# Optimization experiments

Measured on AMD Instinct MI355X. Metric: run time of the kernel, lower is better.

Reference implementation:

```python
import jax, jax.numpy as jnp
import numpy as np

DIM = 512
NUM_HEADS = 8
HEAD_DIM = DIM // NUM_HEADS
LN_EPS = 1e-5


def setup_inputs() -> dict:
    key = jax.random.key(0)
    k1, k2, k3 = jax.random.split(key, 3)
    x = jax.random.normal(k1, (8, DIM, 32, 32), dtype=jnp.float32)
    # torch Linear default init scale ~ 1/sqrt(fan_in); keep values sane
    w_qkv = jax.random.normal(k2, (3 * DIM, DIM), dtype=jnp.float32) * (DIM ** -0.5)
    b_qkv = jax.random.normal(k3, (3 * DIM,), dtype=jnp.float32) * 0.01
    ln_gamma = jnp.ones((DIM,), dtype=jnp.float32)
    ln_beta = jnp.zeros((DIM,), dtype=jnp.float32)
    return {"x": x, "w_qkv": w_qkv, "b_qkv": b_qkv, "ln_gamma": ln_gamma, "ln_beta": ln_beta}


def _rotate_half(t):
    t1, t2 = jnp.split(t, 2, axis=-1)
    return jnp.concatenate((-t2, t1), axis=-1)


def reference(x, w_qkv, b_qkv, ln_gamma, ln_beta):
    B, C, H, W = x.shape
    N = H * W
    nh, hd = NUM_HEADS, HEAD_DIM
    scale = hd ** -0.5

    # [B, N, C]
    xt = x.reshape(B, C, N).transpose(0, 2, 1)

    # LayerNorm over channel dim
    mu = jnp.mean(xt, axis=-1, keepdims=True)
    var = jnp.mean(jnp.square(xt - mu), axis=-1, keepdims=True)
    xn = (xt - mu) * jax.lax.rsqrt(var + LN_EPS) * ln_gamma + ln_beta

    # QKV projection: [B, N, 3C]
    qkv = xn @ w_qkv.T + b_qkv
    qkv = qkv.reshape(B, N, 3, nh, hd).transpose(2, 0, 3, 1, 4)  # [3, B, nh, N, hd]
    q, k, v = qkv[0], qkv[1], qkv[2]

    # RoPE tables
    freqs = 1.0 / (10000.0 ** (jnp.arange(0, hd, 2, dtype=jnp.float32) / hd))
    pos = jnp.arange(N, dtype=jnp.float32)
    sinusoid = jnp.einsum('i,j->ij', pos, freqs)  # [N, hd/2]
    sin = jnp.repeat(jnp.sin(sinusoid), 2, axis=-1)[None, None]  # [1,1,N,hd]
    cos = jnp.repeat(jnp.cos(sinusoid), 2, axis=-1)[None, None]

    q = q * cos + _rotate_half(q) * sin
    k = k * cos + _rotate_half(k) * sin

    # Full softmax attention: [B, nh, N, N]
    attn = jnp.einsum('bhqd,bhkd->bhqk', q, k) * scale
    attn = jax.nn.softmax(attn, axis=-1)
    out = jnp.einsum('bhqk,bhkd->bhqd', attn, v)  # [B, nh, N, hd]

    out = out.transpose(0, 2, 1, 3).reshape(B, N, C)  # [B, N, C]
    # dropout=0 (eval): identity
    return out.transpose(0, 2, 1).reshape(B, C, H, W)
```

## Files before the change

### kernel.cpp

```cpp
#include <hip/hip_runtime.h>
#include <hip/hip_bf16.h>
#include <math.h>

using bf16 = __hip_bfloat16;
typedef __attribute__((ext_vector_type(8))) short short8;
typedef __attribute__((ext_vector_type(4))) short short4_;
typedef __attribute__((ext_vector_type(4))) float floatx4;

#define C_DIM   512
#define N_TOK   1024
#define NHEAD   8
#define HDIM    64
#define LN_EPSF 1e-5f

__device__ __forceinline__ unsigned short f2b(float f) {
    union { float f; unsigned int u; } v; v.f = f;
    unsigned int r = v.u + 0x7FFFu + ((v.u >> 16) & 1u);
    return (unsigned short)(r >> 16);
}
__device__ __forceinline__ float b2f(unsigned short u) {
    union { unsigned int i; float f; } v; v.i = ((unsigned int)u) << 16; return v.f;
}

__global__ __launch_bounds__(256) void prep_kernel(
        const float* __restrict__ x, const float* __restrict__ w,
        float* __restrict__ mu, float* __restrict__ rsig,
        float* __restrict__ sc, unsigned short* __restrict__ wf) {
    __shared__ float red_s[4][64];
    __shared__ float red_q[4][64];
    const int bx = blockIdx.x;
    const int t  = threadIdx.x;
    if (bx < 128) {
        const int rl = t & 63;
        const int cg = t >> 6;
        const int r0 = bx * 64;
        const int b  = r0 >> 10;
        const int n  = (r0 & 1023) + rl;
        const float* xp = x + (size_t)b * C_DIM * N_TOK + n;
        float s = 0.f, q = 0.f;
        #pragma unroll 4
        for (int i = 0; i < 128; ++i) {
            float v = xp[(size_t)(cg * 128 + i) * N_TOK];
            s += v; q += v * v;
        }
        red_s[cg][rl] = s; red_q[cg][rl] = q;
        __syncthreads();
        if (cg == 0) {
            float S = red_s[0][rl] + red_s[1][rl] + red_s[2][rl] + red_s[3][rl];
            float Q = red_q[0][rl] + red_q[1][rl] + red_q[2][rl] + red_q[3][rl];
            float m   = S * (1.0f / C_DIM);
            float var = Q * (1.0f / C_DIM) - m * m;
            mu[r0 + rl]   = m;
            rsig[r0 + rl] = rsqrtf(var + LN_EPSF);
        }
    } else if (bx < 256) {
        const int idx = (bx - 128) * 256 + t;
        const int n = idx >> 5, f = idx & 31;
        const float fr = __expf((float)f * (-9.210340371976184f / 32.0f));
        float sv, cv;
        sincosf((float)n * fr, &sv, &cv);
        ((float2*)sc)[idx] = make_float2(sv, cv);
    } else {
        const int id   = (bx - 256) * 256 + t;
        const int lane = id & 63;
        const int ksl  = (id >> 6) & 15;
        const int j16  = id >> 10;
        const int c    = lane & 15;
        const int quad = lane >> 4;
        const float* wp = w + (size_t)(j16 * 16 + c) * C_DIM + ksl * 32 + quad * 8;
        const float4 w0 = *(const float4*)(wp);
        const float4 w1 = *(const float4*)(wp + 4);
        short8 pk;
        pk[0] = (short)f2b(w0.x); pk[1] = (short)f2b(w0.y);
        pk[2] = (short)f2b(w0.z); pk[3] = (short)f2b(w0.w);
        pk[4] = (short)f2b(w1.x); pk[5] = (short)f2b(w1.y);
        pk[6] = (short)f2b(w1.z); pk[7] = (short)f2b(w1.w);
        *(short8*)(wf + (size_t)id * 8) = pk;
    }
}

__global__ __launch_bounds__(256) void xnt_kernel(
        const float* __restrict__ x, const float* __restrict__ gamma,
        const float* __restrict__ beta, const float* __restrict__ mu,
        const float* __restrict__ rsig, unsigned short* __restrict__ xnf) {
    __shared__ short Sx[64][72];
    const int t  = threadIdx.x;
    const int c0 = blockIdx.x * 64;
    const int n0 = blockIdx.y * 64;
    const int b  = blockIdx.z;

    const int nq  = t & 15;
    const int crl = t >> 4;
    const int tok = b * N_TOK + n0 + nq * 4;
    const float4 m4 = *(const float4*)(mu + tok);
    const float4 r4 = *(const float4*)(rsig + tok);
    #pragma unroll
    for (int p = 0; p < 4; ++p) {
        const int c = c0 + p * 16 + crl;
        const float g = gamma[c], bt = beta[c];
        const float4 xv = *(const float4*)(x + (size_t)b * C_DIM * N_TOK + (size_t)c * N_TOK + n0 + nq * 4);
        Sx[nq * 4 + 0][p * 16 + crl] = (short)f2b((xv.x - m4.x) * r4.x * g + bt);
        Sx[nq * 4 + 1][p * 16 + crl] = (short)f2b((xv.y - m4.y) * r4.y * g + bt);
        Sx[nq * 4 + 2][p * 16 + crl] = (short)f2b((xv.z - m4.z) * r4.z * g + bt);
        Sx[nq * 4 + 3][p * 16 + crl] = (short)f2b((xv.w - m4.w) * r4.w * g + bt);
    }
    __syncthreads();
    const int wv   = t >> 6;
    const int lane = t & 63;
    const int cfr  = lane & 15;
    const int quad = lane >> 4;
    const int g16  = b * 64 + ((n0 >> 4) + wv);
    #pragma unroll
    for (int ks = 0; ks < 2; ++ks) {
        short8 v = *(const short8*)&Sx[wv * 16 + cfr][ks * 32 + quad * 8];
        *(short8*)(xnf + (((size_t)g16 * 16 + (c0 >> 5) + ks) * 64 + lane) * 8) = v;
    }
}

__global__ __launch_bounds__(256) void qkv_mfma_kernel(
        const unsigned short* __restrict__ xnf, const unsigned short* __restrict__ wf,
        const float* __restrict__ bias, const float* __restrict__ sc,
        unsigned short* __restrict__ qfr, unsigned short* __restrict__ kfr,
        unsigned short* __restrict__ vfr) {
    __shared__ short Es[4][64][72];

    const int t    = threadIdx.x;
    const int wv   = t >> 6;
    const int lane = t & 63;
    const int cl   = lane & 15;
    const int quad = lane >> 4;
    const int t0   = blockIdx.x * 128 + (wv & 1) * 64;
    const int j0w  = blockIdx.y * 128 + (wv >> 1) * 64;
    const int which = j0w >> 9;
    const int h     = (j0w >> 6) & 7;
    const int b     = t0 >> 10;
    const int n0q   = t0 & 1023;
    const int bh    = b * NHEAD + h;

    const unsigned short* ap = xnf + (size_t)(t0 >> 4) * 8192 + lane * 8;
    const unsigned short* bp = wf  + (size_t)(j0w >> 4) * 8192 + lane * 8;

    floatx4 acc[4][4];
    #pragma unroll
    for (int i = 0; i < 4; ++i)
        #pragma unroll
        for (int j = 0; j < 4; ++j) acc[i][j] = (floatx4){0.f, 0.f, 0.f, 0.f};

    #pragma unroll 2
    for (int kt = 0; kt < 16; ++kt) {
        short8 af[4], bfr[4];
        #pragma unroll
        for (int tt = 0; tt < 4; ++tt) af[tt]  = *(const short8*)(ap + ((size_t)tt * 16 + kt) * 512);
        #pragma unroll
        for (int jt = 0; jt < 4; ++jt) bfr[jt] = *(const short8*)(bp + ((size_t)jt * 16 + kt) * 512);
        #pragma unroll
        for (int tt = 0; tt < 4; ++tt)
            #pragma unroll
            for (int jt = 0; jt < 4; ++jt)
                acc[tt][jt] = __builtin_amdgcn_mfma_f32_16x16x32_bf16(af[tt], bfr[jt], acc[tt][jt], 0, 0, 0);
    }

    float bj[4];
    #pragma unroll
    for (int jt = 0; jt < 4; ++jt) bj[jt] = bias[j0w + jt * 16 + cl];
    #pragma unroll
    for (int tt = 0; tt < 4; ++tt)
        #pragma unroll
        for (int jt = 0; jt < 4; ++jt)
            #pragma unroll
            for (int r = 0; r < 4; ++r)
                Es[wv][tt * 16 + quad * 4 + r][jt * 16 + cl] = (short)f2b(acc[tt][jt][r] + bj[jt]);

    if (which == 2) {
        unsigned short* vfb = vfr + ((size_t)bh * 16 + (n0q >> 6)) * 4096;
        #pragma unroll
        for (int dt = 0; dt < 4; ++dt) {
            #pragma unroll
            for (int ks = 0; ks < 2; ++ks) {
                short8 pk;
                #pragma unroll
                for (int j = 0; j < 8; ++j)
                    pk[j] = Es[wv][ks * 32 + quad * 8 + j][dt * 16 + cl];
                *(short8*)(vfb + (((size_t)dt * 2 + ks) * 64 + lane) * 8) = pk;
            }
        }
    } else {
        const float oscale = (which == 0) ? 0.125f : 1.0f;
        unsigned short* base = (which == 0)
            ? qfr + ((size_t)bh * 64 + (n0q >> 4)) * 1024
            : kfr + ((size_t)bh * 16 + (n0q >> 6)) * 4096;
        #pragma unroll
        for (int mt = 0; mt < 4; ++mt) {
            const int n = n0q + mt * 16 + cl;
            const float* scp = sc + ((size_t)n * 32 + quad * 4) * 2;
            #pragma unroll
            for (int ks = 0; ks < 2; ++ks) {
                const short8 v8 = *(const short8*)&Es[wv][mt * 16 + cl][ks * 32 + quad * 8];
                const short8 p8 = *(const short8*)&Es[wv][mt * 16 + cl][(ks ^ 1) * 32 + quad * 8];
                const float* sp = scp + ks * 32;
                const float4 s0 = *(const float4*)sp;
                const float4 s1 = *(const float4*)(sp + 4);
                const float sv[4] = {s0.x, s0.z, s1.x, s1.z};
                const float cv[4] = {s0.y, s0.w, s1.y, s1.w};
                const float sgn = ks ? 1.0f : -1.0f;
                short8 pk;
                #pragma unroll
                for (int j = 0; j < 8; ++j) {
                    const int f = j >> 1;
                    const float val = b2f((unsigned short)v8[j]);
                    const float par = b2f((unsigned short)p8[j]);
                    pk[j] = (short)f2b((val * cv[f] + sgn * par * sv[f]) * oscale);
                }
                *(short8*)(base + (((size_t)mt * 2 + ks) * 64 + lane) * 8) = pk;
            }
        }
    }
}

__global__ __launch_bounds__(64, 2) void attn_mfma_kernel(
        const unsigned short* __restrict__ qfr, const unsigned short* __restrict__ kfr,
        const unsigned short* __restrict__ vfr, float* __restrict__ out) {
    __shared__ __align__(16) short Plds[2][16][72];

    const int lane = threadIdx.x;
    const int c    = lane & 15;
    const int quad = lane >> 4;
    const int i    = blockIdx.x;
    const int bh   = (i & 7) * 8 + ((i >> 3) & 7);
    const int qw   = (i >> 6) * 32;
    const int b    = bh >> 3, h = bh & 7;

    const unsigned short* qp = qfr + ((size_t)bh * 64 + (qw >> 4)) * 1024 + lane * 8;
    const unsigned short* kp = kfr + (size_t)bh * 65536 + lane * 8;
    const unsigned short* vp = vfr + (size_t)bh * 65536 + lane * 8;

    short8 qf[2][2];
    #pragma unroll
    for (int qt = 0; qt < 2; ++qt)
        #pragma unroll
        for (int ks = 0; ks < 2; ++ks)
            qf[qt][ks] = *(const short8*)(qp + ((size_t)qt * 2 + ks) * 512);

    floatx4 o_acc[2][4];
    float l_acc[2] = {0.f, 0.f};
    #pragma unroll
    for (int qt = 0; qt < 2; ++qt)
        #pragma unroll
        for (int dt = 0; dt < 4; ++dt) o_acc[qt][dt] = (floatx4){0.f, 0.f, 0.f, 0.f};

    #pragma unroll 1
    for (int kt = 0; kt < 16; ++kt) {
        const unsigned short* kb = kp + (size_t)kt * 4096;
        const unsigned short* vb = vp + (size_t)kt * 4096;
        short8 kf[4][2], vf[4][2];
        #pragma unroll
        for (int mt = 0; mt < 4; ++mt) {
            #pragma unroll
            for (int ks = 0; ks < 2; ++ks) {
                kf[mt][ks] = *(const short8*)(kb + ((size_t)mt * 2 + ks) * 512);
                vf[mt][ks] = *(const short8*)(vb + ((size_t)mt * 2 + ks) * 512);
            }
        }

        floatx4 st[2][4];
        #pragma unroll
        for (int qt = 0; qt < 2; ++qt) {
            #pragma unroll
            for (int mt = 0; mt < 4; ++mt) {
                floatx4 z = (floatx4){0.f, 0.f, 0.f, 0.f};
                z = __builtin_amdgcn_mfma_f32_16x16x32_bf16(kf[mt][0], qf[qt][0], z, 0, 0, 0);
                st[qt][mt] = __builtin_amdgcn_mfma_f32_16x16x32_bf16(kf[mt][1], qf[qt][1], z, 0, 0, 0);
            }
        }

        #pragma unroll
        for (int qt = 0; qt < 2; ++qt) {
            #pragma unroll
            for (int mt = 0; mt < 4; ++mt) {
                const float e0 = __expf(st[qt][mt][0] - 16.0f);
                const float e1 = __expf(st[qt][mt][1] - 16.0f);
                const float e2 = __expf(st[qt][mt][2] - 16.0f);
                const float e3 = __expf(st[qt][mt][3] - 16.0f);
                l_acc[qt] += (e0 + e1) + (e2 + e3);
                short4_ pk;
                pk.x = (short)f2b(e0); pk.y = (short)f2b(e1);
                pk.z = (short)f2b(e2); pk.w = (short)f2b(e3);
                *(short4_*)&Plds[qt][c][mt * 16 + quad * 4] = pk;
            }
        }

        #pragma unroll
        for (int qt = 0; qt < 2; ++qt) {
            const short8 pf0 = *(const short8*)&Plds[qt][c][quad * 8];
            const short8 pf1 = *(const short8*)&Plds[qt][c][32 + quad * 8];
            #pragma unroll
            for (int dt = 0; dt < 4; ++dt) {
                o_acc[qt][dt] = __builtin_amdgcn_mfma_f32_16x16x32_bf16(vf[dt][0], pf0, o_acc[qt][dt], 0, 0, 0);
                o_acc[qt][dt] = __builtin_amdgcn_mfma_f32_16x16x32_bf16(vf[dt][1], pf1, o_acc[qt][dt], 0, 0, 0);
            }
        }
    }

    #pragma unroll
    for (int qt = 0; qt < 2; ++qt) {
        float l = l_acc[qt];
        l += __shfl_xor(l, 16);
        l += __shfl_xor(l, 32);
        const float inv = 1.0f / l;
        const int qcol = qw + qt * 16 + c;
        #pragma unroll
        for (int dt = 0; dt < 4; ++dt) {
            #pragma unroll
            for (int r = 0; r < 4; ++r) {
                const int d = dt * 16 + quad * 4 + r;
                out[((size_t)b * C_DIM + h * HDIM + d) * N_TOK + qcol] = o_acc[qt][dt][r] * inv;
            }
        }
    }
}

extern "C" void kernel_launch(void* const* d_in, const int* in_sizes, int n_in,
                              void* d_out, int out_size, void* d_ws, size_t ws_size,
                              hipStream_t stream) {
    const float* x     = (const float*)d_in[0];
    const float* w     = (const float*)d_in[1];
    const float* bias  = (const float*)d_in[2];
    const float* gamma = (const float*)d_in[3];
    const float* beta  = (const float*)d_in[4];
    float* out = (float*)d_out;

    char* ws = (char*)d_ws;
    float* mu   = (float*)ws;
    float* rsig = (float*)(ws + 32768);
    unsigned short* qfr = (unsigned short*)(ws + 65536);
    unsigned short* kfr = (unsigned short*)(ws + 65536 + 8388608);
    unsigned short* vfr = (unsigned short*)(ws + 65536 + 16777216);
    unsigned short* xnf = (unsigned short*)(ws + 65536 + 25165824);
    unsigned short* wf  = (unsigned short*)(ws + 65536 + 33554432);
    float* sc           = (float*)(ws + 65536 + 35127296);

    hipLaunchKernelGGL(prep_kernel, dim3(640), dim3(256), 0, stream, x, w, mu, rsig, sc, wf);
    hipLaunchKernelGGL(xnt_kernel, dim3(8, 16, 8), dim3(256), 0, stream,
                       x, gamma, beta, mu, rsig, xnf);
    hipLaunchKernelGGL(qkv_mfma_kernel, dim3(64, 12), dim3(256), 0, stream,
                       xnf, wf, bias, sc, qfr, kfr, vfr);
    hipLaunchKernelGGL(attn_mfma_kernel, dim3(2048), dim3(64), 0, stream, qfr, kfr, vfr, out);
}
```

Before: 150.7 us.

## Fuse LayerNorm stats and normalize-transpose into prep kernel; raise attention occupancy hint

The separate xnt kernel is folded into the stats blocks of prep_kernel. Each block computes the mean and rstd for its 64 tokens, keeps them in shared memory, then loops over all 8 channel chunks to write the bf16 fragment layout. This removes a launch and the global mu/rsig round-trip. The cost is that only 128 blocks now do all the normalize work serially, so parallelism for that phase drops. Separately, the attention kernel's launch bounds go from 2 to 3 blocks per SM, which may force register limits or spills.

```diff
diff --git a/kernel.cpp b/kernel.cpp
--- a/kernel.cpp
+++ b/kernel.cpp
@@ -24,34 +24,69 @@
 
 __global__ __launch_bounds__(256) void prep_kernel(
         const float* __restrict__ x, const float* __restrict__ w,
-        float* __restrict__ mu, float* __restrict__ rsig,
-        float* __restrict__ sc, unsigned short* __restrict__ wf) {
-    __shared__ float red_s[4][64];
-    __shared__ float red_q[4][64];
+        const float* __restrict__ gamma, const float* __restrict__ beta,
+        float* __restrict__ sc, unsigned short* __restrict__ xnf,
+        unsigned short* __restrict__ wf) {
     const int bx = blockIdx.x;
     const int t  = threadIdx.x;
     if (bx < 128) {
-        const int rl = t & 63;
-        const int cg = t >> 6;
-        const int r0 = bx * 64;
-        const int b  = r0 >> 10;
-        const int n  = (r0 & 1023) + rl;
-        const float* xp = x + (size_t)b * C_DIM * N_TOK + n;
-        float s = 0.f, q = 0.f;
-        #pragma unroll 4
-        for (int i = 0; i < 128; ++i) {
-            float v = xp[(size_t)(cg * 128 + i) * N_TOK];
-            s += v; q += v * v;
-        }
-        red_s[cg][rl] = s; red_q[cg][rl] = q;
-        __syncthreads();
-        if (cg == 0) {
-            float S = red_s[0][rl] + red_s[1][rl] + red_s[2][rl] + red_s[3][rl];
-            float Q = red_q[0][rl] + red_q[1][rl] + red_q[2][rl] + red_q[3][rl];
-            float m   = S * (1.0f / C_DIM);
-            float var = Q * (1.0f / C_DIM) - m * m;
-            mu[r0 + rl]   = m;
-            rsig[r0 + rl] = rsqrtf(var + LN_EPSF);
+        __shared__ float red_s[4][64];
+        __shared__ float red_q[4][64];
+        __shared__ float lmu[64];
+        __shared__ float lrs[64];
+        __shared__ short Sx[64][72];
+        const int b  = bx >> 4;
+        const int n0 = (bx & 15) * 64;
+        {
+            const int rl = t & 63;
+            const int cg = t >> 6;
+            const float* xp = x + (size_t)b * C_DIM * N_TOK + n0 + rl;
+            float s = 0.f, q = 0.f;
+            #pragma unroll 4
+            for (int i = 0; i < 128; ++i) {
+                float v = xp[(size_t)(cg * 128 + i) * N_TOK];
+                s += v; q += v * v;
+            }
+            red_s[cg][rl] = s; red_q[cg][rl] = q;
+            __syncthreads();
+            if (cg == 0) {
+                float S = red_s[0][rl] + red_s[1][rl] + red_s[2][rl] + red_s[3][rl];
+                float Q = red_q[0][rl] + red_q[1][rl] + red_q[2][rl] + red_q[3][rl];
+                float m   = S * (1.0f / C_DIM);
+                float var = Q * (1.0f / C_DIM) - m * m;
+                lmu[rl] = m;
+                lrs[rl] = rsqrtf(var + LN_EPSF);
+            }
+            __syncthreads();
+        }
+        const int nq  = t & 15;
+        const int crl = t >> 4;
+        const int wv   = t >> 6;
+        const int lane = t & 63;
+        const int cfr  = lane & 15;
+        const int quad = lane >> 4;
+        const int g16  = b * 64 + (n0 >> 4) + wv;
+        const float4 m4 = *(const float4*)&lmu[nq * 4];
+        const float4 r4 = *(const float4*)&lrs[nq * 4];
+        for (int cc = 0; cc < 8; ++cc) {
+            const int c0 = cc * 64;
+            #pragma unroll
+            for (int p = 0; p < 4; ++p) {
+                const int c = c0 + p * 16 + crl;
+                const float g = gamma[c], bt = beta[c];
+                const float4 xv = *(const float4*)(x + (size_t)b * C_DIM * N_TOK + (size_t)c * N_TOK + n0 + nq * 4);
+                Sx[nq * 4 + 0][p * 16 + crl] = (short)f2b((xv.x - m4.x) * r4.x * g + bt);
+                Sx[nq * 4 + 1][p * 16 + crl] = (short)f2b((xv.y - m4.y) * r4.y * g + bt);
+                Sx[nq * 4 + 2][p * 16 + crl] = (short)f2b((xv.z - m4.z) * r4.z * g + bt);
+                Sx[nq * 4 + 3][p * 16 + crl] = (short)f2b((xv.w - m4.w) * r4.w * g + bt);
+            }
+            __syncthreads();
+            #pragma unroll
+            for (int ks = 0; ks < 2; ++ks) {
+                short8 v = *(const short8*)&Sx[wv * 16 + cfr][ks * 32 + quad * 8];
+                *(short8*)(xnf + (((size_t)g16 * 16 + cc * 2 + ks) * 64 + lane) * 8) = v;
+            }
+            __syncthreads();
         }
     } else if (bx < 256) {
         const int idx = (bx - 128) * 256 + t;
@@ -79,44 +114,6 @@
     }
 }
 
-__global__ __launch_bounds__(256) void xnt_kernel(
-        const float* __restrict__ x, const float* __restrict__ gamma,
-        const float* __restrict__ beta, const float* __restrict__ mu,
-        const float* __restrict__ rsig, unsigned short* __restrict__ xnf) {
-    __shared__ short Sx[64][72];
-    const int t  = threadIdx.x;
-    const int c0 = blockIdx.x * 64;
-    const int n0 = blockIdx.y * 64;
-    const int b  = blockIdx.z;
-
-    const int nq  = t & 15;
-    const int crl = t >> 4;
-    const int tok = b * N_TOK + n0 + nq * 4;
-    const float4 m4 = *(const float4*)(mu + tok);
-    const float4 r4 = *(const float4*)(rsig + tok);
-    #pragma unroll
-    for (int p = 0; p < 4; ++p) {
-        const int c = c0 + p * 16 + crl;
-        const float g = gamma[c], bt = beta[c];
-        const float4 xv = *(const float4*)(x + (size_t)b * C_DIM * N_TOK + (size_t)c * N_TOK + n0 + nq * 4);
-        Sx[nq * 4 + 0][p * 16 + crl] = (short)f2b((xv.x - m4.x) * r4.x * g + bt);
-        Sx[nq * 4 + 1][p * 16 + crl] = (short)f2b((xv.y - m4.y) * r4.y * g + bt);
-        Sx[nq * 4 + 2][p * 16 + crl] = (short)f2b((xv.z - m4.z) * r4.z * g + bt);
-        Sx[nq * 4 + 3][p * 16 + crl] = (short)f2b((xv.w - m4.w) * r4.w * g + bt);
-    }
-    __syncthreads();
-    const int wv   = t >> 6;
-    const int lane = t & 63;
-    const int cfr  = lane & 15;
-    const int quad = lane >> 4;
-    const int g16  = b * 64 + ((n0 >> 4) + wv);
-    #pragma unroll
-    for (int ks = 0; ks < 2; ++ks) {
-        short8 v = *(const short8*)&Sx[wv * 16 + cfr][ks * 32 + quad * 8];
-        *(short8*)(xnf + (((size_t)g16 * 16 + (c0 >> 5) + ks) * 64 + lane) * 8) = v;
-    }
-}
-
 __global__ __launch_bounds__(256) void qkv_mfma_kernel(
         const unsigned short* __restrict__ xnf, const unsigned short* __restrict__ wf,
         const float* __restrict__ bias, const float* __restrict__ sc,
@@ -217,7 +214,7 @@
     }
 }
 
-__global__ __launch_bounds__(64, 2) void attn_mfma_kernel(
+__global__ __launch_bounds__(64, 3) void attn_mfma_kernel(
         const unsigned short* __restrict__ qfr, const unsigned short* __restrict__ kfr,
         const unsigned short* __restrict__ vfr, float* __restrict__ out) {
     __shared__ __align__(16) short Plds[2][16][72];
@@ -227,10 +224,10 @@
     const int quad = lane >> 4;
     const int i    = blockIdx.x;
     const int bh   = (i & 7) * 8 + ((i >> 3) & 7);
-    const int qw   = (i >> 6) * 32;
+    const int q32  = i >> 6;
     const int b    = bh >> 3, h = bh & 7;
 
-    const unsigned short* qp = qfr + ((size_t)bh * 64 + (qw >> 4)) * 1024 + lane * 8;
+    const unsigned short* qp = qfr + ((size_t)bh * 64 + q32 * 2) * 1024 + lane * 8;
     const unsigned short* kp = kfr + (size_t)bh * 65536 + lane * 8;
     const unsigned short* vp = vfr + (size_t)bh * 65536 + lane * 8;
 
@@ -307,7 +304,7 @@
         l += __shfl_xor(l, 16);
         l += __shfl_xor(l, 32);
         const float inv = 1.0f / l;
-        const int qcol = qw + qt * 16 + c;
+        const int qcol = q32 * 32 + qt * 16 + c;
         #pragma unroll
         for (int dt = 0; dt < 4; ++dt) {
             #pragma unroll
@@ -330,18 +327,15 @@
     float* out = (float*)d_out;
 
     char* ws = (char*)d_ws;
-    float* mu   = (float*)ws;
-    float* rsig = (float*)(ws + 32768);
-    unsigned short* qfr = (unsigned short*)(ws + 65536);
-    unsigned short* kfr = (unsigned short*)(ws + 65536 + 8388608);
-    unsigned short* vfr = (unsigned short*)(ws + 65536 + 16777216);
-    unsigned short* xnf = (unsigned short*)(ws + 65536 + 25165824);
-    unsigned short* wf  = (unsigned short*)(ws + 65536 + 33554432);
-    float* sc           = (float*)(ws + 65536 + 35127296);
-
-    hipLaunchKernelGGL(prep_kernel, dim3(640), dim3(256), 0, stream, x, w, mu, rsig, sc, wf);
-    hipLaunchKernelGGL(xnt_kernel, dim3(8, 16, 8), dim3(256), 0, stream,
-                       x, gamma, beta, mu, rsig, xnf);
+    unsigned short* qfr = (unsigned short*)ws;
+    unsigned short* kfr = (unsigned short*)(ws + 8388608);
+    unsigned short* vfr = (unsigned short*)(ws + 16777216);
+    unsigned short* xnf = (unsigned short*)(ws + 25165824);
+    unsigned short* wf  = (unsigned short*)(ws + 33554432);
+    float* sc           = (float*)(ws + 35127296);
+
+    hipLaunchKernelGGL(prep_kernel, dim3(640), dim3(256), 0, stream,
+                       x, w, gamma, beta, sc, xnf, wf);
     hipLaunchKernelGGL(qkv_mfma_kernel, dim3(64, 12), dim3(256), 0, stream,
                        xnf, wf, bias, sc, qfr, kfr, vfr);
     hipLaunchKernelGGL(attn_mfma_kernel, dim3(2048), dim3(64), 0, stream, qfr, kfr, vfr, out);
```

New measurement: 151.8 us. No clear change (+0.8%).
